# Kernel tuning notes

Measured on AMD Instinct MI355X. Metric: run time of the kernel, lower is better.

The kernel has to match this reference:

```python
import jax, jax.numpy as jnp
import numpy as np

B, L, D = 4, 4096, 1024
DS, EXP, DC = 16, 2, 4
DI = EXP * D
K_SYM = max(3, 2 * DC + 1)  # 9


def _linear(x, w, b):
    # torch nn.Linear: y = x @ W^T + b, W:[out,in]
    return jnp.einsum('blc,oc->blo', x, w) + b


def _dwconv(x, kernel, bias, pad_l, pad_r):
    # x:[B,L,C], kernel:[C,1,k] depthwise, torch 'same' padding (asymmetric for even k)
    y = jax.lax.conv_general_dilated(
        x.transpose(0, 2, 1), kernel, window_strides=(1,),
        padding=[(pad_l, pad_r)], dimension_numbers=('NCH', 'OIH', 'NCH'),
        feature_group_count=x.shape[-1])
    return y.transpose(0, 2, 1) + bias


def _rmsnorm(x, w, eps=1e-6):
    scale = jax.lax.rsqrt(jnp.mean(x * x, axis=-1, keepdims=True) + eps)
    return w * x * scale


def setup_inputs() -> dict:
    key = jax.random.key(0)
    ks = jax.random.split(key, 12)
    def n(k, shape, s=0.02):
        return jax.random.normal(k, shape, jnp.float32) * s
    return {
        'x': jax.random.normal(ks[0], (B, L, D), jnp.float32),
        'norm_w': jnp.ones((D,), jnp.float32),
        'in_w': n(ks[1], (2 * DI, D)), 'in_b': jnp.zeros((2 * DI,), jnp.float32),
        'dwa_k': n(ks[2], (DI, 1, DC)), 'dwa_b': jnp.zeros((DI,), jnp.float32),
        'A': n(ks[3], (DI, DS)), 'Bm': n(ks[4], (DS, DI)),
        'sym_k': n(ks[5], (DI, 1, K_SYM)), 'sym_b': jnp.zeros((DI,), jnp.float32),
        'pw_w': n(ks[6], (DI, DI)), 'pw_b': jnp.zeros((DI,), jnp.float32),
        'ha_w': n(ks[7], (DI // 2, DI)), 'ha_b': jnp.zeros((DI // 2,), jnp.float32),
        'hb_w': n(ks[8], (DI // 2, DI)), 'hb_b': jnp.zeros((DI // 2,), jnp.float32),
        'fuse_w': n(ks[9], (DI, DI)), 'fuse_b': jnp.zeros((DI,), jnp.float32),
        'out_w': n(ks[10], (D, DI)), 'out_b': jnp.zeros((D,), jnp.float32),
    }


def reference(x, norm_w, in_w, in_b, dwa_k, dwa_b, A, Bm, sym_k, sym_b,
              pw_w, pw_b, ha_w, ha_b, hb_w, hb_b, fuse_w, fuse_b, out_w, out_b):
    residual = x
    h = _rmsnorm(x, norm_w)
    h = _linear(h, in_w, in_b)                       # [B,L,2*DI]
    gate, val = h[..., :DI], h[..., DI:]
    gate = jax.nn.sigmoid(gate)
    # mamba-like branch: depthwise conv (k=4, torch 'same' -> pad (1,2)) + low-rank A@B
    a = _dwconv(val, dwa_k, dwa_b, 1, 2)             # [B,L,DI]
    a = jnp.einsum('bld,ds->bls', a, A)              # [B,L,DS]
    a = jnp.einsum('bls,sd->bld', a, Bm)             # [B,L,DI]
    # symmetric conv branch: depthwise conv (k=9, pad (4,4)) -> silu -> pointwise linear
    b = _dwconv(val, sym_k, sym_b, K_SYM // 2, K_SYM // 2)
    b = jax.nn.silu(b)
    b = _linear(b, pw_w, pw_b)
    a = _linear(a, ha_w, ha_b)                       # [B,L,DI/2]
    b = _linear(b, hb_w, hb_b)                       # [B,L,DI/2]
    y = jnp.concatenate([a, b], axis=-1)             # [B,L,DI]
    y = _linear(y, fuse_w, fuse_b)
    y = gate * y
    y = _linear(y, out_w, out_b)                     # [B,L,D]
    return residual + y
```

## Files before the change

### kernel.cpp

```cpp
#include <hip/hip_runtime.h>
#include <hip/hip_bf16.h>
#include <stdint.h>

typedef __bf16 bf16;
typedef __bf16 bf16x8 __attribute__((ext_vector_type(8)));
typedef __bf16 bf16x4 __attribute__((ext_vector_type(4)));
typedef float  f32x4  __attribute__((ext_vector_type(4)));

#define LDS_PTR(p) ((__attribute__((address_space(3))) uint32_t*)(p))
#define GLB_PTR(p) ((const __attribute__((address_space(1))) uint32_t*)(p))

static constexpr int BATCH = 4, SEQ = 4096, DMODEL = 1024;
static constexpr int DI = 2048;
static constexpr int MTOK = BATCH * SEQ;

enum { EPI_SPLIT = 0, EPI_PLAIN = 1, EPI_ZGATE = 2, EPI_RES = 3, EPI_F32S = 4 };

template <int EPI, bool SPLITK = false>
__global__ __launch_bounds__(256) void gemm_bt(
    const bf16* __restrict__ Aact, const bf16* __restrict__ W,
    const float* __restrict__ bias,
    bf16* __restrict__ out0, bf16* __restrict__ out1,
    const bf16* __restrict__ gate,
    float* __restrict__ outf, const float* __restrict__ resid,
    int N, int K, int ldC, int col_off)
{
  __shared__ __align__(16) bf16 sA[128 * 64];
  __shared__ __align__(16) bf16 sB[128 * 64];
  const int tid  = threadIdx.x;
  int n0, m0, kbeg, kend;
  size_t out_off = 0;
  if (SPLITK) {
    n0 = blockIdx.z * 128;
    m0 = blockIdx.y * 128;
    const int kh = K / gridDim.x;
    kbeg = blockIdx.x * kh; kend = kbeg + kh;
    out_off = (EPI == EPI_F32S) ? (size_t)blockIdx.x * (size_t)col_off
                                : (size_t)blockIdx.x * ((size_t)MTOK * 128);
  } else {
    const int nT  = gridDim.x;
    const int lin = blockIdx.y * nT + blockIdx.x;
    const int grp = lin / (8 * nT);
    const int within = lin - grp * (8 * nT);
    n0 = (within >> 3) * 128;
    m0 = (grp * 8 + (within & 7)) * 128;
    kbeg = 0; kend = K;
  }
  const int lane = tid & 63;
  const int wv   = tid >> 6;
  const int wr   = wv >> 1, wc = wv & 1;
  const int l15  = lane & 15, quad = lane >> 4;

  f32x4 acc[4][4];
#pragma unroll
  for (int i = 0; i < 4; ++i)
#pragma unroll
    for (int j = 0; j < 4; ++j) acc[i][j] = (f32x4){0.f, 0.f, 0.f, 0.f};

  int rr[4], cb[4];
#pragma unroll
  for (int j = 0; j < 4; ++j) {
    const int s = tid + j * 256;
    rr[j] = s >> 3;
    cb[j] = ((s & 7) ^ (rr[j] & 7)) * 16;
  }

  const char* gA = (const char*)(Aact + (size_t)m0 * K);
  const char* gW = (const char*)(W + (size_t)n0 * K);

  for (int k0 = kbeg; k0 < kend; k0 += 64) {
    if (k0 != kbeg) __syncthreads();
#pragma unroll
    for (int j = 0; j < 4; ++j)
      __builtin_amdgcn_global_load_lds(GLB_PTR(gA + ((size_t)rr[j] * K + k0) * 2 + cb[j]),
                                       LDS_PTR(sA + (tid + j * 256) * 8), 16, 0, 0);
#pragma unroll
    for (int j = 0; j < 4; ++j)
      __builtin_amdgcn_global_load_lds(GLB_PTR(gW + ((size_t)rr[j] * K + k0) * 2 + cb[j]),
                                       LDS_PTR(sB + (tid + j * 256) * 8), 16, 0, 0);
    __syncthreads();

#pragma unroll
    for (int h = 0; h < 2; ++h) {
      bf16x8 av[4], bv[4];
#pragma unroll
      for (int t = 0; t < 4; ++t) {
        const int Ra = wr * 64 + t * 16 + l15;
        const int Rb = wc * 64 + t * 16 + l15;
        const int cc = h * 4 + quad;
        av[t] = *(const bf16x8*)(sA + (Ra * 8 + (cc ^ (Ra & 7))) * 8);
        bv[t] = *(const bf16x8*)(sB + (Rb * 8 + (cc ^ (Rb & 7))) * 8);
      }
#pragma unroll
      for (int i = 0; i < 4; ++i)
#pragma unroll
        for (int j = 0; j < 4; ++j)
          acc[i][j] = __builtin_amdgcn_mfma_f32_16x16x32_bf16(av[i], bv[j], acc[i][j], 0, 0, 0);
    }
  }

  float* sS = (float*)sA;
  float* sT = (float*)sB;
  float tt[4][16];
  if (EPI == EPI_ZGATE) {
    __syncthreads();
    const float* s16f = outf;
    const float* T2   = resid;
    {
      const float4 a0 = ((const float4*)(s16f + (size_t)m0 * 16))[tid * 2];
      const float4 a1 = ((const float4*)(s16f + (size_t)m0 * 16))[tid * 2 + 1];
      const float4 b0 = ((const float4*)(T2 + (size_t)n0 * 16))[tid * 2];
      const float4 b1 = ((const float4*)(T2 + (size_t)n0 * 16))[tid * 2 + 1];
      const int i0 = tid * 8;
      const float av_[8] = {a0.x, a0.y, a0.z, a0.w, a1.x, a1.y, a1.z, a1.w};
      const float bv_[8] = {b0.x, b0.y, b0.z, b0.w, b1.x, b1.y, b1.z, b1.w};
#pragma unroll
      for (int e = 0; e < 8; ++e) {
        const int idx = i0 + e;
        sS[(idx >> 4) * 17 + (idx & 15)] = av_[e];
        sT[(idx >> 4) * 17 + (idx & 15)] = bv_[e];
      }
    }
    __syncthreads();
#pragma unroll
    for (int j = 0; j < 4; ++j) {
      const int nloc = wc * 64 + j * 16 + l15;
#pragma unroll
      for (int s = 0; s < 16; ++s) tt[j][s] = sT[nloc * 17 + s];
    }
  }

  bf16*  o0 = out0 + out_off;
  float* of = outf ? outf + out_off : nullptr;
#pragma unroll
  for (int i = 0; i < 4; ++i) {
    const int mbase = m0 + wr * 64 + i * 16 + quad * 4;
#pragma unroll
    for (int r = 0; r < 4; ++r) {
      const int mm = mbase + r;
      float sv[16];
      if (EPI == EPI_ZGATE) {
        const int mloc = wr * 64 + i * 16 + quad * 4 + r;
#pragma unroll
        for (int s = 0; s < 16; ++s) sv[s] = sS[mloc * 17 + s];
      }
#pragma unroll
      for (int j = 0; j < 4; ++j) {
        const int n = n0 + wc * 64 + j * 16 + l15;
        const float bj = bias ? bias[n] : 0.f;
        float v = acc[i][j][r] + bj;
        if (EPI == EPI_SPLIT) {
          if (n < DI) o0[(size_t)mm * DI + n] = (bf16)(1.f / (1.f + __expf(-v)));
          else        out1[(size_t)mm * DI + (n - DI)] = (bf16)v;
        } else if (EPI == EPI_PLAIN) {
          o0[(size_t)mm * ldC + col_off + n] = (bf16)v;
        } else if (EPI == EPI_ZGATE) {
#pragma unroll
          for (int s = 0; s < 16; ++s) v += sv[s] * tt[j][s];
          const float g = (float)gate[(size_t)mm * DI + n];
          o0[(size_t)mm * ldC + n] = (bf16)(v * g);
        } else if (EPI == EPI_F32S) {
          of[(size_t)mm * ldC + n] = v;
        } else {
          outf[(size_t)mm * ldC + n] = v + resid[(size_t)mm * ldC + n];
        }
      }
    }
  }
}

__global__ __launch_bounds__(256) void rmsnorm_kernel(
    const float* __restrict__ x, const float* __restrict__ w, bf16* __restrict__ out)
{
  const int row = blockIdx.x;
  const int tid = threadIdx.x;
  const float4 xv = ((const float4*)(x + (size_t)row * DMODEL))[tid];
  float s = xv.x * xv.x + xv.y * xv.y + xv.z * xv.z + xv.w * xv.w;
#pragma unroll
  for (int o = 32; o; o >>= 1) s += __shfl_xor(s, o);
  __shared__ float red[4];
  if ((tid & 63) == 0) red[tid >> 6] = s;
  __syncthreads();
  const float tot = red[0] + red[1] + red[2] + red[3];
  const float scale = rsqrtf(tot * (1.f / DMODEL) + 1e-6f);
  const float4 wv = ((const float4*)w)[tid];
  bf16x4 o4 = { (bf16)(xv.x * wv.x * scale), (bf16)(xv.y * wv.y * scale),
                (bf16)(xv.z * wv.z * scale), (bf16)(xv.w * wv.w * scale) };
  *(bf16x4*)(out + (size_t)row * DMODEL + tid * 4) = o4;
}

static constexpr int TL2 = 32;
__global__ __launch_bounds__(256) void conv_kernel(
    const bf16* __restrict__ val,
    const float* __restrict__ sym_k, const float* __restrict__ sym_b,
    bf16* __restrict__ bbuf)
{
  const int d  = (blockIdx.y * 256 + threadIdx.x) * 4;
  const int b  = blockIdx.z;
  const int l0 = blockIdx.x * TL2;
  float wk[9][4], bs[4];
#pragma unroll
  for (int j = 0; j < 4; ++j) {
    bs[j] = sym_b[d + j];
#pragma unroll
    for (int k = 0; k < 9; ++k) wk[k][j] = sym_k[(d + j) * 9 + k];
  }
  const bf16* base = val + (size_t)b * SEQ * DI + d;

  float win[9][4];
#pragma unroll
  for (int j = 0; j < 8; ++j) {
    const int xr = l0 + j - 4;
    if (xr >= 0 && xr < SEQ) {
      bf16x4 v = *(const bf16x4*)(base + (size_t)xr * DI);
#pragma unroll
      for (int c = 0; c < 4; ++c) win[j][c] = (float)v[c];
    } else {
#pragma unroll
      for (int c = 0; c < 4; ++c) win[j][c] = 0.f;
    }
  }
  for (int t = 0; t < TL2; ++t) {
    const int xf = l0 + t + 4;
    if (xf < SEQ) {
      bf16x4 v = *(const bf16x4*)(base + (size_t)xf * DI);
#pragma unroll
      for (int c = 0; c < 4; ++c) win[8][c] = (float)v[c];
    } else {
#pragma unroll
      for (int c = 0; c < 4; ++c) win[8][c] = 0.f;
    }
    float sb[4];
#pragma unroll
    for (int c = 0; c < 4; ++c) sb[c] = bs[c];
#pragma unroll
    for (int k = 0; k < 9; ++k)
#pragma unroll
      for (int c = 0; c < 4; ++c) sb[c] += win[k][c] * wk[k][c];
    bf16x4 o;
#pragma unroll
    for (int c = 0; c < 4; ++c) o[c] = (bf16)(sb[c] / (1.f + __expf(-sb[c])));
    *(bf16x4*)(bbuf + ((size_t)b * SEQ + l0 + t) * DI + d) = o;
#pragma unroll
    for (int k = 0; k < 8; ++k)
#pragma unroll
      for (int c = 0; c < 4; ++c) win[k][c] = win[k + 1][c];
  }
}

__global__ __launch_bounds__(256) void prep_cvt_kernel(
    const float* __restrict__ in_w, const float* __restrict__ hb_w,
    const float* __restrict__ out_w, const float* __restrict__ pw_w,
    bf16* __restrict__ in_wbf, bf16* __restrict__ hb_bf,
    bf16* __restrict__ out_bf, bf16* __restrict__ pwT_bf)
{
  __shared__ float s[32][33];
  const int b = blockIdx.x;
  const int tid = threadIdx.x;
  if (b < 8192) {
    const float* src; bf16* dst; size_t i;
    if (b < 4096)      { src = in_w;  dst = in_wbf; i = (size_t)b * 256 + tid; }
    else if (b < 6144) { src = hb_w;  dst = hb_bf;  i = (size_t)(b - 4096) * 256 + tid; }
    else               { src = out_w; dst = out_bf; i = (size_t)(b - 6144) * 256 + tid; }
    const float4 v = ((const float4*)src)[i];
    bf16x4 o4 = { (bf16)v.x, (bf16)v.y, (bf16)v.z, (bf16)v.w };
    *(bf16x4*)(dst + 4 * i) = o4;
  } else {
    const int q = b - 8192;
    const int d0 = (q & 63) * 32, c0 = (q >> 6) * 32;
    const int r = tid >> 5, x = tid & 31;
#pragma unroll
    for (int rr = r; rr < 32; rr += 8)
      s[rr][x] = pw_w[(size_t)(c0 + rr) * 2048 + d0 + x];
    __syncthreads();
#pragma unroll
    for (int rr = r; rr < 32; rr += 8)
      pwT_bf[(size_t)(d0 + rr) * 2048 + c0 + x] = (bf16)s[x][rr];
  }
}

__global__ __launch_bounds__(256) void prep_small_kernel(
    const float* __restrict__ Bm, const float* __restrict__ ha_w,
    const float* __restrict__ dwa_b, const float* __restrict__ dwa_k,
    const float* __restrict__ A,
    const float* __restrict__ hb_w, const float* __restrict__ pw_b,
    const float* __restrict__ hb_b, const float* __restrict__ fuse_w,
    const float* __restrict__ Hp,
    float* __restrict__ T1, float* __restrict__ cvec, float* __restrict__ b_H,
    bf16* __restrict__ Wp, bf16* __restrict__ Fb, bf16* __restrict__ Ht)
{
  const int b = blockIdx.x, tid = threadIdx.x;
  __shared__ float red[4][16];
  if (b < 1024) {
    const int o = b;
    float acc[16];
#pragma unroll
    for (int s = 0; s < 16; ++s) acc[s] = 0.f;
    for (int d = tid; d < 2048; d += 256) {
      const float w = ha_w[(size_t)o * 2048 + d];
#pragma unroll
      for (int s = 0; s < 16; ++s) acc[s] += Bm[s * 2048 + d] * w;
    }
    const int lane = tid & 63, wv = tid >> 6;
#pragma unroll
    for (int s = 0; s < 16; ++s) {
      float v = acc[s];
#pragma unroll
      for (int off = 32; off; off >>= 1) v += __shfl_xor(v, off);
      if (lane == s) red[wv][s] = v;
    }
    __syncthreads();
    if (tid < 16)
      T1[tid * 1024 + o] = red[0][tid] + red[1][tid] + red[2][tid] + red[3][tid];
  } else if (b == 1024) {
    float acc[16];
#pragma unroll
    for (int s = 0; s < 16; ++s) acc[s] = 0.f;
    for (int d = tid; d < 2048; d += 256) {
      const float w = dwa_b[d];
#pragma unroll
      for (int s = 0; s < 16; ++s) acc[s] += w * A[d * 16 + s];
    }
    const int lane = tid & 63, wv = tid >> 6;
#pragma unroll
    for (int s = 0; s < 16; ++s) {
      float v = acc[s];
#pragma unroll
      for (int off = 32; off; off >>= 1) v += __shfl_xor(v, off);
      if (lane == s) red[wv][s] = v;
    }
    __syncthreads();
    if (tid < 16) cvec[tid] = red[0][tid] + red[1][tid] + red[2][tid] + red[3][tid];
  } else if (b < 1029) {
    const int o = (b - 1025) * 256 + tid;
    float acc = hb_b[o];
    const float* hr = hb_w + (size_t)o * 2048;
    for (int c = 0; c < 2048; c += 4) {
      float4 h = *(const float4*)(hr + c);
      float4 p = *(const float4*)(pw_b + c);
      acc += h.x * p.x + h.y * p.y + h.z * p.z + h.w * p.w;
    }
    b_H[o] = acc;
  } else if (b < 1037) {
    const int d = (b - 1029) * 256 + tid;
    float kk[4], av[16];
#pragma unroll
    for (int k = 0; k < 4; ++k) kk[k] = dwa_k[d * 4 + k];
#pragma unroll
    for (int s = 0; s < 16; ++s) av[s] = A[d * 16 + s];
#pragma unroll
    for (int k = 0; k < 4; ++k)
#pragma unroll
      for (int s = 0; s < 16; ++s)
        Wp[(size_t)(k * 16 + s) * 2048 + d] = (bf16)(kk[k] * av[s]);
    for (int n = 64; n < 128; ++n) Wp[(size_t)n * 2048 + d] = (bf16)0.f;
  } else if (b < 3085) {
    const int idx = (b - 1037) * 256 + tid;
    const int n = idx >> 8, o4 = idx & 255;
    float4 v = ((const float4*)(fuse_w + (size_t)n * 2048 + 1024))[o4];
    bf16x4 o = { (bf16)v.x, (bf16)v.y, (bf16)v.z, (bf16)v.w };
    *(bf16x4*)(Fb + (size_t)n * 1024 + o4 * 4) = o;
  } else {
    const size_t e4 = (size_t)(b - 3085) * 256 + tid;
    float4 p0 = ((const float4*)Hp)[e4];
    float4 p1 = ((const float4*)(Hp + 2048 * 1024))[e4];
    bf16x4 o = { (bf16)(p0.x + p1.x), (bf16)(p0.y + p1.y),
                 (bf16)(p0.z + p1.z), (bf16)(p0.w + p1.w) };
    *(bf16x4*)(Ht + e4 * 4) = o;
  }
}

__global__ __launch_bounds__(256) void prep_fuse_kernel(
    const float* __restrict__ T1, const float* __restrict__ fuse_w,
    const float* __restrict__ fuse_b, const float* __restrict__ ha_b,
    const float* __restrict__ b_H,
    float* __restrict__ T2t, float* __restrict__ bias_z)
{
  const int b = blockIdx.x, tid = threadIdx.x;
  if (b < 128) {
    const int n = b * 16 + (tid >> 4);
    const int s = tid & 15;
    const float* fr = fuse_w + (size_t)n * 2048;
    const float* tr = T1 + s * 1024;
    float acc = 0.f;
    for (int o = 0; o < 1024; o += 4) {
      float4 f = *(const float4*)(fr + o);
      float4 t = *(const float4*)(tr + o);
      acc += f.x * t.x + f.y * t.y + f.z * t.z + f.w * t.w;
    }
    T2t[n * 16 + s] = acc;
  } else {
    const int n = b - 128;
    const float* fr = fuse_w + (size_t)n * 2048;
    const int o = tid * 4;
    float4 fa = *(const float4*)(fr + o);
    float4 fb = *(const float4*)(fr + 1024 + o);
    float4 ha = *(const float4*)(ha_b + o);
    float4 bh = *(const float4*)(b_H + o);
    float acc = fa.x * ha.x + fa.y * ha.y + fa.z * ha.z + fa.w * ha.w
              + fb.x * bh.x + fb.y * bh.y + fb.z * bh.z + fb.w * bh.w;
#pragma unroll
    for (int off = 32; off; off >>= 1) acc += __shfl_xor(acc, off);
    __shared__ float r4[4];
    if ((tid & 63) == 0) r4[tid >> 6] = acc;
    __syncthreads();
    if (tid == 0) bias_z[n] = fuse_b[n] + r4[0] + r4[1] + r4[2] + r4[3];
  }
}

__global__ __launch_bounds__(256) void s16_kernel(
    const bf16* __restrict__ P0, const bf16* __restrict__ P1,
    const float* __restrict__ cvec, float* __restrict__ s16f)
{
  const int g = blockIdx.x * 256 + threadIdx.x;
  const int tok = g >> 4, s = g & 15;
  const int l = tok & (SEQ - 1), bb = tok >> 12;
  float acc = cvec[s];
#pragma unroll
  for (int k = 0; k < 4; ++k) {
    const int r = l - 1 + k;
    if ((unsigned)r < (unsigned)SEQ) {
      const size_t idx = ((size_t)bb * SEQ + r) * 128 + k * 16 + s;
      acc += (float)P0[idx] + (float)P1[idx];
    }
  }
  s16f[(size_t)tok * 16 + s] = acc;
}

extern "C" void kernel_launch(void* const* d_in, const int* in_sizes, int n_in,
                              void* d_out, int out_size, void* d_ws, size_t ws_size,
                              hipStream_t stream)
{
  const float* x      = (const float*)d_in[0];
  const float* norm_w = (const float*)d_in[1];
  const float* in_w   = (const float*)d_in[2];
  const float* in_b   = (const float*)d_in[3];
  const float* dwa_k  = (const float*)d_in[4];
  const float* dwa_b  = (const float*)d_in[5];
  const float* Amat   = (const float*)d_in[6];
  const float* Bm     = (const float*)d_in[7];
  const float* sym_k  = (const float*)d_in[8];
  const float* sym_b  = (const float*)d_in[9];
  const float* pw_w   = (const float*)d_in[10];
  const float* pw_b   = (const float*)d_in[11];
  const float* ha_w   = (const float*)d_in[12];
  const float* ha_b   = (const float*)d_in[13];
  const float* hb_w   = (const float*)d_in[14];
  const float* hb_b   = (const float*)d_in[15];
  const float* fuse_w = (const float*)d_in[16];
  const float* fuse_b = (const float*)d_in[17];
  const float* out_w  = (const float*)d_in[18];
  const float* out_b  = (const float*)d_in[19];
  float* out = (float*)d_out;

  char* ws = (char*)d_ws;
  const size_t MB = 1u << 20, KB = 1u << 10;
  bf16*  in_wbf  = (bf16*)(ws + 0);
  bf16*  hnorm   = (bf16*)(ws + 8 * MB);
  bf16*  bsilu   = (bf16*)(ws + 0);
  float* Hpart   = (float*)(ws + 64 * MB);
  bf16*  valp    = (bf16*)(ws + 64 * MB);
  bf16*  zbuf    = (bf16*)(ws + 64 * MB);
  bf16*  gatep   = (bf16*)(ws + 128 * MB);
  bf16*  Pbuf    = (bf16*)(ws + 192 * MB);
  bf16*  pwT_bf  = (bf16*)(ws + 200 * MB);
  bf16*  WB_bf   = (bf16*)(ws + 200 * MB);
  bf16*  hb_bf   = (bf16*)(ws + 208 * MB);
  bf16*  Fb_bf   = (bf16*)(ws + 208 * MB);
  float* s16f    = (float*)(ws + 208 * MB);
  bf16*  Ht_bf   = (bf16*)(ws + 212 * MB);
  bf16*  out_bf  = (bf16*)(ws + 216 * MB);
  float* T1      = (float*)(ws + 220 * MB);
  float* cvec    = (float*)(ws + 220 * MB + 64 * KB);
  float* b_H     = (float*)(ws + 220 * MB + 68 * KB);
  float* bias_z  = (float*)(ws + 220 * MB + 72 * KB);
  bf16*  Wp      = (bf16*)(ws + 220 * MB + 80 * KB);
  float* T2t     = (float*)(ws + 220 * MB + 592 * KB);

  prep_cvt_kernel<<<12288, 256, 0, stream>>>(
      in_w, hb_w, out_w, pw_w, in_wbf, hb_bf, out_bf, pwT_bf);
  gemm_bt<EPI_F32S, true><<<dim3(2, 16, 8), 256, 0, stream>>>(
      pwT_bf, hb_bf, nullptr, nullptr, nullptr, nullptr, Hpart, nullptr,
      1024, 2048, 1024, 2048 * 1024);
  prep_small_kernel<<<5133, 256, 0, stream>>>(
      Bm, ha_w, dwa_b, dwa_k, Amat, hb_w, pw_b, hb_b, fuse_w, Hpart,
      T1, cvec, b_H, Wp, Fb_bf, Ht_bf);
  gemm_bt<EPI_PLAIN><<<dim3(16, 16), 256, 0, stream>>>(
      Fb_bf, Ht_bf, nullptr, WB_bf, nullptr, nullptr, nullptr, nullptr, 2048, 1024, 2048, 0);
  prep_fuse_kernel<<<2176, 256, 0, stream>>>(T1, fuse_w, fuse_b, ha_b, b_H, T2t, bias_z);

  rmsnorm_kernel<<<MTOK, 256, 0, stream>>>(x, norm_w, hnorm);
  gemm_bt<EPI_SPLIT><<<dim3(32, 128), 256, 0, stream>>>(
      hnorm, in_wbf, in_b, gatep, valp, nullptr, nullptr, nullptr, 4096, 1024, DI, 0);
  conv_kernel<<<dim3(SEQ / TL2, 2, BATCH), 256, 0, stream>>>(
      valp, sym_k, sym_b, bsilu);
  gemm_bt<EPI_PLAIN, true><<<dim3(2, 128), 256, 0, stream>>>(
      valp, Wp, nullptr, Pbuf, nullptr, nullptr, nullptr, nullptr, 128, 2048, 128, 0);
  s16_kernel<<<MTOK * 16 / 256, 256, 0, stream>>>(
      Pbuf, Pbuf + (size_t)MTOK * 128, cvec, s16f);
  gemm_bt<EPI_ZGATE><<<dim3(16, 128), 256, 0, stream>>>(
      bsilu, WB_bf, bias_z, zbuf, nullptr, gatep, s16f, T2t, 2048, 2048, 2048, 0);
  gemm_bt<EPI_RES><<<dim3(8, 128), 256, 0, stream>>>(
      zbuf, out_bf, out_b, nullptr, nullptr, nullptr, out, x, 1024, 2048, 1024, 0);
}
```

Baseline: 949.8 us.

## Fold rank-16 correction into GEMM as extra zero-padded bf16 K tile

The rank-16 update (s16 × T2) was previously done in the ZGATE epilogue with an fp32 LDS staging pass and 16 FMAs per output element. It is now expressed as one extra 64-wide K tile: s16 and T2 are written as bf16 with 48 zero-padded columns, and the tile is appended to the main GEMM loop so the MFMAs handle it. This removes the epilogue LDS traffic, two barriers and the scalar FMA work. In exchange it costs one extra MFMA tile, and the correction terms lose precision because they are now stored in bf16 instead of fp32. The epilogue loop order is also swapped so the bias load is hoisted per column.

New measurement: 836.7 us. -11.9%, faster.

```diff
diff --git a/kernel.cpp b/kernel.cpp
--- a/kernel.cpp
+++ b/kernel.cpp
@@ -14,16 +14,17 @@
 static constexpr int DI = 2048;
 static constexpr int MTOK = BATCH * SEQ;
 
-enum { EPI_SPLIT = 0, EPI_PLAIN = 1, EPI_ZGATE = 2, EPI_RES = 3, EPI_F32S = 4 };
-
-template <int EPI, bool SPLITK = false>
+enum { EPI_SPLIT = 0, EPI_PLAIN = 1, EPI_GATE = 2, EPI_RES = 3, EPI_F32S = 4 };
+
+template <int EPI, bool SPLITK = false, bool KEXT = false>
 __global__ __launch_bounds__(256) void gemm_bt(
     const bf16* __restrict__ Aact, const bf16* __restrict__ W,
     const float* __restrict__ bias,
     bf16* __restrict__ out0, bf16* __restrict__ out1,
     const bf16* __restrict__ gate,
     float* __restrict__ outf, const float* __restrict__ resid,
-    int N, int K, int ldC, int col_off)
+    int N, int K, int ldC, int col_off,
+    const bf16* __restrict__ Ax, const bf16* __restrict__ Bx)
 {
   __shared__ __align__(16) bf16 sA[128 * 64];
   __shared__ __align__(16) bf16 sB[128 * 64];
@@ -68,16 +69,30 @@
   const char* gA = (const char*)(Aact + (size_t)m0 * K);
   const char* gW = (const char*)(W + (size_t)n0 * K);
 
-  for (int k0 = kbeg; k0 < kend; k0 += 64) {
-    if (k0 != kbeg) __syncthreads();
-#pragma unroll
-    for (int j = 0; j < 4; ++j)
-      __builtin_amdgcn_global_load_lds(GLB_PTR(gA + ((size_t)rr[j] * K + k0) * 2 + cb[j]),
-                                       LDS_PTR(sA + (tid + j * 256) * 8), 16, 0, 0);
-#pragma unroll
-    for (int j = 0; j < 4; ++j)
-      __builtin_amdgcn_global_load_lds(GLB_PTR(gW + ((size_t)rr[j] * K + k0) * 2 + cb[j]),
-                                       LDS_PTR(sB + (tid + j * 256) * 8), 16, 0, 0);
+  const int ntile = (kend - kbeg) >> 6;
+  const int ttot  = KEXT ? ntile + 1 : ntile;
+  for (int ti = 0; ti < ttot; ++ti) {
+    if (ti) __syncthreads();
+    if (!KEXT || ti < ntile) {
+      const int k0 = kbeg + ti * 64;
+#pragma unroll
+      for (int j = 0; j < 4; ++j)
+        __builtin_amdgcn_global_load_lds(GLB_PTR(gA + ((size_t)rr[j] * K + k0) * 2 + cb[j]),
+                                         LDS_PTR(sA + (tid + j * 256) * 8), 16, 0, 0);
+#pragma unroll
+      for (int j = 0; j < 4; ++j)
+        __builtin_amdgcn_global_load_lds(GLB_PTR(gW + ((size_t)rr[j] * K + k0) * 2 + cb[j]),
+                                         LDS_PTR(sB + (tid + j * 256) * 8), 16, 0, 0);
+    } else {
+#pragma unroll
+      for (int j = 0; j < 4; ++j)
+        __builtin_amdgcn_global_load_lds(GLB_PTR((const char*)Ax + ((size_t)(m0 + rr[j]) * 64) * 2 + cb[j]),
+                                         LDS_PTR(sA + (tid + j * 256) * 8), 16, 0, 0);
+#pragma unroll
+      for (int j = 0; j < 4; ++j)
+        __builtin_amdgcn_global_load_lds(GLB_PTR((const char*)Bx + ((size_t)(n0 + rr[j]) * 64) * 2 + cb[j]),
+                                         LDS_PTR(sB + (tid + j * 256) * 8), 16, 0, 0);
+    }
     __syncthreads();
 
 #pragma unroll
@@ -99,64 +114,25 @@
     }
   }
 
-  float* sS = (float*)sA;
-  float* sT = (float*)sB;
-  float tt[4][16];
-  if (EPI == EPI_ZGATE) {
-    __syncthreads();
-    const float* s16f = outf;
-    const float* T2   = resid;
-    {
-      const float4 a0 = ((const float4*)(s16f + (size_t)m0 * 16))[tid * 2];
-      const float4 a1 = ((const float4*)(s16f + (size_t)m0 * 16))[tid * 2 + 1];
-      const float4 b0 = ((const float4*)(T2 + (size_t)n0 * 16))[tid * 2];
-      const float4 b1 = ((const float4*)(T2 + (size_t)n0 * 16))[tid * 2 + 1];
-      const int i0 = tid * 8;
-      const float av_[8] = {a0.x, a0.y, a0.z, a0.w, a1.x, a1.y, a1.z, a1.w};
-      const float bv_[8] = {b0.x, b0.y, b0.z, b0.w, b1.x, b1.y, b1.z, b1.w};
-#pragma unroll
-      for (int e = 0; e < 8; ++e) {
-        const int idx = i0 + e;
-        sS[(idx >> 4) * 17 + (idx & 15)] = av_[e];
-        sT[(idx >> 4) * 17 + (idx & 15)] = bv_[e];
-      }
-    }
-    __syncthreads();
-#pragma unroll
-    for (int j = 0; j < 4; ++j) {
-      const int nloc = wc * 64 + j * 16 + l15;
-#pragma unroll
-      for (int s = 0; s < 16; ++s) tt[j][s] = sT[nloc * 17 + s];
-    }
-  }
-
   bf16*  o0 = out0 + out_off;
   float* of = outf ? outf + out_off : nullptr;
 #pragma unroll
   for (int i = 0; i < 4; ++i) {
     const int mbase = m0 + wr * 64 + i * 16 + quad * 4;
 #pragma unroll
-    for (int r = 0; r < 4; ++r) {
-      const int mm = mbase + r;
-      float sv[16];
-      if (EPI == EPI_ZGATE) {
-        const int mloc = wr * 64 + i * 16 + quad * 4 + r;
-#pragma unroll
-        for (int s = 0; s < 16; ++s) sv[s] = sS[mloc * 17 + s];
-      }
-#pragma unroll
-      for (int j = 0; j < 4; ++j) {
-        const int n = n0 + wc * 64 + j * 16 + l15;
-        const float bj = bias ? bias[n] : 0.f;
+    for (int j = 0; j < 4; ++j) {
+      const int n = n0 + wc * 64 + j * 16 + l15;
+      const float bj = bias ? bias[n] : 0.f;
+#pragma unroll
+      for (int r = 0; r < 4; ++r) {
+        const int mm = mbase + r;
         float v = acc[i][j][r] + bj;
         if (EPI == EPI_SPLIT) {
           if (n < DI) o0[(size_t)mm * DI + n] = (bf16)(1.f / (1.f + __expf(-v)));
           else        out1[(size_t)mm * DI + (n - DI)] = (bf16)v;
         } else if (EPI == EPI_PLAIN) {
           o0[(size_t)mm * ldC + col_off + n] = (bf16)v;
-        } else if (EPI == EPI_ZGATE) {
-#pragma unroll
-          for (int s = 0; s < 16; ++s) v += sv[s] * tt[j][s];
+        } else if (EPI == EPI_GATE) {
           const float g = (float)gate[(size_t)mm * DI + n];
           o0[(size_t)mm * ldC + n] = (bf16)(v * g);
         } else if (EPI == EPI_F32S) {
@@ -374,7 +350,7 @@
     const float* __restrict__ T1, const float* __restrict__ fuse_w,
     const float* __restrict__ fuse_b, const float* __restrict__ ha_b,
     const float* __restrict__ b_H,
-    float* __restrict__ T2t, float* __restrict__ bias_z)
+    bf16* __restrict__ T2e, float* __restrict__ bias_z)
 {
   const int b = blockIdx.x, tid = threadIdx.x;
   if (b < 128) {
@@ -388,7 +364,10 @@
       float4 t = *(const float4*)(tr + o);
       acc += f.x * t.x + f.y * t.y + f.z * t.z + f.w * t.w;
     }
-    T2t[n * 16 + s] = acc;
+    T2e[(size_t)n * 64 + s]      = (bf16)acc;
+    T2e[(size_t)n * 64 + s + 16] = (bf16)0.f;
+    T2e[(size_t)n * 64 + s + 32] = (bf16)0.f;
+    T2e[(size_t)n * 64 + s + 48] = (bf16)0.f;
   } else {
     const int n = b - 128;
     const float* fr = fuse_w + (size_t)n * 2048;
@@ -410,7 +389,7 @@
 
 __global__ __launch_bounds__(256) void s16_kernel(
     const bf16* __restrict__ P0, const bf16* __restrict__ P1,
-    const float* __restrict__ cvec, float* __restrict__ s16f)
+    const float* __restrict__ cvec, bf16* __restrict__ s16e)
 {
   const int g = blockIdx.x * 256 + threadIdx.x;
   const int tok = g >> 4, s = g & 15;
@@ -424,7 +403,10 @@
       acc += (float)P0[idx] + (float)P1[idx];
     }
   }
-  s16f[(size_t)tok * 16 + s] = acc;
+  s16e[(size_t)tok * 64 + s]      = (bf16)acc;
+  s16e[(size_t)tok * 64 + s + 16] = (bf16)0.f;
+  s16e[(size_t)tok * 64 + s + 32] = (bf16)0.f;
+  s16e[(size_t)tok * 64 + s + 48] = (bf16)0.f;
 }
 
 extern "C" void kernel_launch(void* const* d_in, const int* in_sizes, int n_in,
@@ -467,7 +449,7 @@
   bf16*  WB_bf   = (bf16*)(ws + 200 * MB);
   bf16*  hb_bf   = (bf16*)(ws + 208 * MB);
   bf16*  Fb_bf   = (bf16*)(ws + 208 * MB);
-  float* s16f    = (float*)(ws + 208 * MB);
+  bf16*  s16e    = (bf16*)(ws + 208 * MB);
   bf16*  Ht_bf   = (bf16*)(ws + 212 * MB);
   bf16*  out_bf  = (bf16*)(ws + 216 * MB);
   float* T1      = (float*)(ws + 220 * MB);
@@ -475,31 +457,36 @@
   float* b_H     = (float*)(ws + 220 * MB + 68 * KB);
   float* bias_z  = (float*)(ws + 220 * MB + 72 * KB);
   bf16*  Wp      = (bf16*)(ws + 220 * MB + 80 * KB);
-  float* T2t     = (float*)(ws + 220 * MB + 592 * KB);
+  bf16*  T2e     = (bf16*)(ws + 220 * MB + 592 * KB);
 
   prep_cvt_kernel<<<12288, 256, 0, stream>>>(
       in_w, hb_w, out_w, pw_w, in_wbf, hb_bf, out_bf, pwT_bf);
   gemm_bt<EPI_F32S, true><<<dim3(2, 16, 8), 256, 0, stream>>>(
       pwT_bf, hb_bf, nullptr, nullptr, nullptr, nullptr, Hpart, nullptr,
-      1024, 2048, 1024, 2048 * 1024);
+      1024, 2048, 1024, 2048 * 1024, nullptr, nullptr);
   prep_small_kernel<<<5133, 256, 0, stream>>>(
       Bm, ha_w, dwa_b, dwa_k, Amat, hb_w, pw_b, hb_b, fuse_w, Hpart,
       T1, cvec, b_H, Wp, Fb_bf, Ht_bf);
   gemm_bt<EPI_PLAIN><<<dim3(16, 16), 256, 0, stream>>>(
-      Fb_bf, Ht_bf, nullptr, WB_bf, nullptr, nullptr, nullptr, nullptr, 2048, 1024, 2048, 0);
-  prep_fuse_kernel<<<2176, 256, 0, stream>>>(T1, fuse_w, fuse_b, ha_b, b_H, T2t, bias_z);
+      Fb_bf, Ht_bf, nullptr, WB_bf, nullptr, nullptr, nullptr, nullptr,
+      2048, 1024, 2048, 0, nullptr, nullptr);
+  prep_fuse_kernel<<<2176, 256, 0, stream>>>(T1, fuse_w, fuse_b, ha_b, b_H, T2e, bias_z);
 
   rmsnorm_kernel<<<MTOK, 256, 0, stream>>>(x, norm_w, hnorm);
   gemm_bt<EPI_SPLIT><<<dim3(32, 128), 256, 0, stream>>>(
-      hnorm, in_wbf, in_b, gatep, valp, nullptr, nullptr, nullptr, 4096, 1024, DI, 0);
+      hnorm, in_wbf, in_b, gatep, valp, nullptr, nullptr, nullptr,
+      4096, 1024, DI, 0, nullptr, nullptr);
   conv_kernel<<<dim3(SEQ / TL2, 2, BATCH), 256, 0, stream>>>(
       valp, sym_k, sym_b, bsilu);
   gemm_bt<EPI_PLAIN, true><<<dim3(2, 128), 256, 0, stream>>>(
-      valp, Wp, nullptr, Pbuf, nullptr, nullptr, nullptr, nullptr, 128, 2048, 128, 0);
+      valp, Wp, nullptr, Pbuf, nullptr, nullptr, nullptr, nullptr,
+      128, 2048, 128, 0, nullptr, nullptr);
   s16_kernel<<<MTOK * 16 / 256, 256, 0, stream>>>(
-      Pbuf, Pbuf + (size_t)MTOK * 128, cvec, s16f);
-  gemm_bt<EPI_ZGATE><<<dim3(16, 128), 256, 0, stream>>>(
-      bsilu, WB_bf, bias_z, zbuf, nullptr, gatep, s16f, T2t, 2048, 2048, 2048, 0);
+      Pbuf, Pbuf + (size_t)MTOK * 128, cvec, s16e);
+  gemm_bt<EPI_GATE, false, true><<<dim3(16, 128), 256, 0, stream>>>(
+      bsilu, WB_bf, bias_z, zbuf, nullptr, gatep, nullptr, nullptr,
+      2048, 2048, 2048, 0, s16e, T2e);
   gemm_bt<EPI_RES><<<dim3(8, 128), 256, 0, stream>>>(
-      zbuf, out_bf, out_b, nullptr, nullptr, nullptr, out, x, 1024, 2048, 1024, 0);
-}
+      zbuf, out_bf, out_b, nullptr, nullptr, nullptr, out, x,
+      1024, 2048, 1024, 0, nullptr, nullptr);
+}
```
